# Performance work log

Measured on AMD Instinct MI355X. Metric: run time of the kernel, lower is better.

The kernel has to match this reference:

```python
import jax, jax.numpy as jnp
import numpy as np
from jax import lax

GROUPS = 8
EPS = 1e-5

def setup_inputs() -> dict:
    key = jax.random.key(0)
    ks = jax.random.split(key, 4)
    B, C, H, W = 32, 256, 64, 64
    cg = C // GROUPS  # 32 channels per group
    x = jax.random.normal(ks[0], (B, C, H, W), dtype=jnp.float32)
    w1 = jax.random.normal(ks[1], (cg, cg, 1, 1), dtype=jnp.float32) * 0.02  # conv1x1 OIHW
    b1 = jnp.zeros((cg,), jnp.float32)
    w3 = jax.random.normal(ks[2], (cg, cg, 3, 3), dtype=jnp.float32) * 0.02  # conv3x3 OIHW
    b3 = jnp.zeros((cg,), jnp.float32)
    gn_w = jnp.ones((cg,), jnp.float32)
    gn_b = jnp.zeros((cg,), jnp.float32)
    return {"x": x, "w1": w1, "b1": b1, "w3": w3, "b3": b3, "gn_w": gn_w, "gn_b": gn_b}

def reference(x, w1, b1, w3, b3, gn_w, gn_b):
    B, C, H, W = x.shape
    cg = C // GROUPS
    bg = B * GROUPS
    gx = x.reshape(bg, cg, H, W)

    # coordinate pooling: (bg,cg,H,1) and (bg,cg,W,1)
    x_h = jnp.mean(gx, axis=3, keepdims=True)
    x_w = jnp.mean(gx, axis=2, keepdims=True).transpose(0, 1, 3, 2)

    # 1x1 conv over concatenated coord features (bg,cg,H+W,1)
    hw = jnp.einsum('bihk,oi->bohk', jnp.concatenate([x_h, x_w], axis=2), w1[:, :, 0, 0])
    hw = hw + b1[None, :, None, None]
    xh, xw = hw[:, :, :H, :], hw[:, :, H:, :]

    # sigmoid coordinate gating
    gated = gx * jax.nn.sigmoid(xh) * jax.nn.sigmoid(xw.transpose(0, 1, 3, 2))

    # GroupNorm(cg groups over cg channels) == per-channel instance norm over HxW
    mu = jnp.mean(gated, axis=(2, 3), keepdims=True)
    var = jnp.var(gated, axis=(2, 3), keepdims=True)
    x1 = (gated - mu) * lax.rsqrt(var + EPS)
    x1 = x1 * gn_w[None, :, None, None] + gn_b[None, :, None, None]

    # 3x3 conv branch
    x2 = lax.conv_general_dilated(gx, w3, (1, 1), 'SAME',
                                  dimension_numbers=('NCHW', 'OIHW', 'NCHW'))
    x2 = x2 + b3[None, :, None, None]

    # cross-branch attention weights
    x11 = jax.nn.softmax(jnp.mean(x1, axis=(2, 3)), axis=-1)[:, None, :]  # (bg,1,cg)
    x21 = jax.nn.softmax(jnp.mean(x2, axis=(2, 3)), axis=-1)[:, None, :]  # (bg,1,cg)
    x12 = x2.reshape(bg, cg, H * W)
    x22 = x1.reshape(bg, cg, H * W)
    weights = (jnp.matmul(x11, x12) + jnp.matmul(x21, x22)).reshape(bg, 1, H, W)

    out = (gx * jax.nn.sigmoid(weights)).reshape(B, C, H, W) + x
    return out
```

## Files before the change

kernel.cpp:

```cpp
#include <hip/hip_runtime.h>
#include <math.h>

#define NPLANE 8192
#define PLANE  4096

__device__ __forceinline__ float sigm(float v){ return 1.0f/(1.0f+expf(-v)); }

__global__ __launch_bounds__(256) void kA(const float* __restrict__ x,
                                          float* __restrict__ rowsum,
                                          float* __restrict__ colsum,
                                          float* __restrict__ corners){
  const int plane = blockIdx.x;
  const float* __restrict__ p = x + (size_t)plane*PLANE;
  const int t = threadIdx.x;
  __shared__ float cpart[256][4];
  __shared__ float rsh[64];
  float ca0=0.f, ca1=0.f, ca2=0.f, ca3=0.f;
  #pragma unroll
  for(int iter=0; iter<4; ++iter){
    const int flat = iter*1024 + t*4;
    const float4 v = *reinterpret_cast<const float4*>(p + flat);
    float rp = v.x+v.y+v.z+v.w;
    #pragma unroll
    for(int s=1;s<16;s<<=1) rp += __shfl_xor(rp, s, 64);
    if((t&15)==0) rsh[flat>>6] = rp;
    ca0+=v.x; ca1+=v.y; ca2+=v.z; ca3+=v.w;
    if(iter==0 && t==0)   corners[(size_t)plane*4+0]=v.x;
    if(iter==0 && t==15)  corners[(size_t)plane*4+1]=v.w;
    if(iter==3 && t==240) corners[(size_t)plane*4+2]=v.x;
    if(iter==3 && t==255) corners[(size_t)plane*4+3]=v.w;
  }
  cpart[t][0]=ca0; cpart[t][1]=ca1; cpart[t][2]=ca2; cpart[t][3]=ca3;
  __syncthreads();
  if(t<64){
    const int g=t>>2, j=t&3;
    float s=0.f;
    #pragma unroll
    for(int k=0;k<16;++k) s += cpart[g + k*16][j];
    colsum[(size_t)plane*64 + t] = s;
    rowsum[(size_t)plane*64 + t] = rsh[t];
  }
}

__global__ __launch_bounds__(256) void kB0(const float* __restrict__ gn_b,
                                           const float* __restrict__ w3,
                                           const float* __restrict__ b3,
                                           float* __restrict__ wcg,
                                           float* __restrict__ cbg){
  __shared__ float x11[32];
  const int t=threadIdx.x;
  if(t==0){
    float m=-1e30f;
    #pragma unroll
    for(int c=0;c<32;++c) m=fmaxf(m,gn_b[c]);
    float e[32]; float s=0.f;
    #pragma unroll
    for(int c=0;c<32;++c){ e[c]=expf(gn_b[c]-m); s+=e[c]; }
    const float inv=1.f/s;
    float cb=0.f;
    #pragma unroll
    for(int c=0;c<32;++c){ x11[c]=e[c]*inv; cb+=x11[c]*b3[c]; }
    *cbg=cb;
  }
  __syncthreads();
  for(int idx=t; idx<288; idx+=256){
    const int i=idx/9, k=idx%9;
    float s=0.f;
    #pragma unroll
    for(int c=0;c<32;++c) s += x11[c]*w3[(c*32+i)*9+k];
    wcg[idx]=s;
  }
}

__global__ __launch_bounds__(256) void kB(const float* __restrict__ rowsum,
                                          const float* __restrict__ colsum,
                                          const float* __restrict__ corners,
                                          const float* __restrict__ w1,
                                          const float* __restrict__ b1,
                                          const float* __restrict__ w3,
                                          const float* __restrict__ b3,
                                          float* __restrict__ sh,
                                          float* __restrict__ sw,
                                          float* __restrict__ x21){
  const int b = blockIdx.x;
  const int t = threadIdx.x;
  __shared__ float m[32][128];
  __shared__ float w1s[1024];
  __shared__ float S[32][9];
  __shared__ float mean2[32];
  const float* __restrict__ rs = rowsum + (size_t)b*32*64;
  const float* __restrict__ cs = colsum + (size_t)b*32*64;
  for(int idx=t; idx<2048; idx+=256){
    m[idx>>6][idx&63]        = rs[idx]*(1.0f/64.0f);
    m[idx>>6][64+(idx&63)]   = cs[idx]*(1.0f/64.0f);
  }
  for(int idx=t; idx<1024; idx+=256) w1s[idx]=w1[idx];
  __syncthreads();
  {
    const int o = t>>3;
    const int p0 = (t&7)<<4;
    const float bias = b1[o];
    #pragma unroll
    for(int pp=0;pp<16;++pp){
      const int p = p0+pp;
      float acc = bias;
      #pragma unroll
      for(int i=0;i<32;++i) acc += w1s[o*32+i]*m[i][p];
      const float sg = sigm(acc);
      if(p<64) sh[((size_t)b*32+o)*64 + p]      = sg;
      else     sw[((size_t)b*32+o)*64 + (p-64)] = sg;
    }
  }
  if(t<32){
    const int i=t;
    float Ti=0.f;
    #pragma unroll
    for(int h=0;h<64;++h) Ti += m[i][h];
    Ti *= 64.f;
    const float r0=m[i][0]*64.f, r63=m[i][63]*64.f;
    const float c0=m[i][64]*64.f, c63=m[i][127]*64.f;
    const float* cr = corners + ((size_t)b*32+i)*4;
    const float k00=cr[0], k01=cr[1], k10=cr[2], k11=cr[3];
    #pragma unroll
    for(int ky=0;ky<3;++ky){
      #pragma unroll
      for(int kx=0;kx<3;++kx){
        float s=Ti;
        if(ky==0) s-=r63; else if(ky==2) s-=r0;
        if(kx==0) s-=c63; else if(kx==2) s-=c0;
        if(ky==0&&kx==0) s+=k11;
        if(ky==0&&kx==2) s+=k10;
        if(ky==2&&kx==0) s+=k01;
        if(ky==2&&kx==2) s+=k00;
        S[i][ky*3+kx]=s;
      }
    }
  }
  __syncthreads();
  if(t<32){
    const int c=t;
    float acc=0.f;
    for(int i=0;i<32;++i){
      #pragma unroll
      for(int k=0;k<9;++k) acc += w3[(c*32+i)*9+k]*S[i][k];
    }
    mean2[c] = acc*(1.0f/4096.0f) + b3[c];
  }
  __syncthreads();
  if(t==0){
    float mx=-1e30f;
    #pragma unroll
    for(int c=0;c<32;++c) mx=fmaxf(mx,mean2[c]);
    float e[32]; float s=0.f;
    #pragma unroll
    for(int c=0;c<32;++c){ e[c]=expf(mean2[c]-mx); s+=e[c]; }
    const float inv=1.f/s;
    #pragma unroll
    for(int c=0;c<32;++c) x21[(size_t)b*32+c]=e[c]*inv;
  }
}

__global__ __launch_bounds__(256) void kC(const float* __restrict__ x,
                                          const float* __restrict__ sh,
                                          const float* __restrict__ sw,
                                          float* __restrict__ musum,
                                          float* __restrict__ sqsum){
  const int plane = blockIdx.x;
  const int t = threadIdx.x;
  const float* __restrict__ p = x + (size_t)plane*PLANE;
  __shared__ float shs[64], sws[64];
  if(t<64){ shs[t]=sh[(size_t)plane*64+t]; sws[t]=sw[(size_t)plane*64+t]; }
  __syncthreads();
  float s=0.f, q=0.f;
  #pragma unroll
  for(int iter=0;iter<4;++iter){
    const int flat=iter*1024 + t*4;
    const float4 v = *reinterpret_cast<const float4*>(p+flat);
    const int row=flat>>6, col=flat&63;
    const float a=shs[row];
    const float g0=v.x*a*sws[col+0], g1=v.y*a*sws[col+1];
    const float g2=v.z*a*sws[col+2], g3=v.w*a*sws[col+3];
    s += g0+g1+g2+g3;
    q += g0*g0+g1*g1+g2*g2+g3*g3;
  }
  #pragma unroll
  for(int sft=1;sft<64;sft<<=1){ s+=__shfl_xor(s,sft,64); q+=__shfl_xor(q,sft,64); }
  __shared__ float rsum[4], rsq[4];
  if((t&63)==0){ rsum[t>>6]=s; rsq[t>>6]=q; }
  __syncthreads();
  if(t==0){ musum[plane]=rsum[0]+rsum[1]+rsum[2]+rsum[3];
            sqsum[plane]=rsq[0]+rsq[1]+rsq[2]+rsq[3]; }
}

__global__ __launch_bounds__(256) void kE(const float* __restrict__ x,
    const float* __restrict__ sh, const float* __restrict__ sw,
    const float* __restrict__ x21, const float* __restrict__ musum,
    const float* __restrict__ sqsum, const float* __restrict__ gn_w,
    const float* __restrict__ gn_b, const float* __restrict__ wc,
    const float* __restrict__ cb, float* __restrict__ out){
  const int b = blockIdx.x>>2;
  const int tile0 = (blockIdx.x&3)<<4;
  const int t = threadIdx.x;
  __shared__ float Lbuf[18][66];
  __shared__ float shs[32][16];
  __shared__ float sws[32][64];
  __shared__ float alphas[32];
  __shared__ float wcs[288];
  __shared__ float constsh;

  if(t<32){
    const float ms = musum[(size_t)b*32+t]*(1.0f/4096.0f);
    const float vv = sqsum[(size_t)b*32+t]*(1.0f/4096.0f) - ms*ms;
    const float rq = rsqrtf(vv + 1e-5f);
    const float xv = x21[(size_t)b*32+t];
    alphas[t] = xv*gn_w[t]*rq;
    float part = xv*(gn_b[t] - gn_w[t]*rq*ms);
    #pragma unroll
    for(int s=1;s<32;s<<=1) part += __shfl_xor(part, s, 64);
    if(t==0) constsh = part + cb[0];
  }
  for(int idx=t; idx<288; idx+=256) wcs[idx]=wc[idx];
  for(int idx=t; idx<512; idx+=256){
    const int i=idx>>4, r=idx&15;
    shs[i][r] = sh[((size_t)b*32+i)*64 + tile0 + r];
  }
  for(int idx=t; idx<2048; idx+=256){
    const int i=idx>>6, w=idx&63;
    sws[i][w] = sw[((size_t)b*32+i)*64 + w];
  }
  if(t<18){ Lbuf[t][0]=0.f; Lbuf[t][65]=0.f; }

  const int r  = t>>4;
  const int c0 = (t&15)<<2;
  float wacc0=0.f, wacc1=0.f, wacc2=0.f, wacc3=0.f;

  for(int i=0;i<32;++i){
    const float* __restrict__ p = x + ((size_t)b*32+i)*(size_t)PLANE;
    __syncthreads();
    for(int idx=t; idx<288; idx+=256){
      const int rr=idx>>4, c4=(idx&15)<<2;
      const int gr=tile0+rr-1;
      float4 v = make_float4(0.f,0.f,0.f,0.f);
      if(gr>=0 && gr<64) v = *reinterpret_cast<const float4*>(p + gr*64 + c4);
      Lbuf[rr][c4+1]=v.x; Lbuf[rr][c4+2]=v.y; Lbuf[rr][c4+3]=v.z; Lbuf[rr][c4+4]=v.w;
    }
    __syncthreads();
    const float q0=wcs[i*9+0], q1=wcs[i*9+1], q2=wcs[i*9+2];
    const float q3=wcs[i*9+3], q4=wcs[i*9+4], q5=wcs[i*9+5];
    const float q6=wcs[i*9+6], q7=wcs[i*9+7], q8=wcs[i*9+8];
    const float ash = alphas[i]*shs[i][r];
    #pragma unroll
    for(int j=0;j<4;++j){
      const int cc=c0+j+1;
      const float a0=Lbuf[r  ][cc-1], a1=Lbuf[r  ][cc], a2=Lbuf[r  ][cc+1];
      const float e0=Lbuf[r+1][cc-1], e1=Lbuf[r+1][cc], e2=Lbuf[r+1][cc+1];
      const float d0=Lbuf[r+2][cc-1], d1=Lbuf[r+2][cc], d2=Lbuf[r+2][cc+1];
      float acc = q0*a0+q1*a1+q2*a2 + q3*e0+q4*e1+q5*e2 + q6*d0+q7*d1+q8*d2;
      acc += ash*sws[i][c0+j]*e1;
      if(j==0) wacc0+=acc; else if(j==1) wacc1+=acc;
      else if(j==2) wacc2+=acc; else wacc3+=acc;
    }
  }
  __syncthreads();
  const float cst = constsh;
  const float wf0 = 1.f + sigm(wacc0+cst);
  const float wf1 = 1.f + sigm(wacc1+cst);
  const float wf2 = 1.f + sigm(wacc2+cst);
  const float wf3 = 1.f + sigm(wacc3+cst);
  const size_t rowoff = (size_t)(tile0+r)*64 + c0;
  for(int i=0;i<32;++i){
    const size_t off = ((size_t)b*32+i)*(size_t)PLANE + rowoff;
    const float4 v = *reinterpret_cast<const float4*>(x + off);
    float4 o;
    o.x=v.x*wf0; o.y=v.y*wf1; o.z=v.z*wf2; o.w=v.w*wf3;
    *reinterpret_cast<float4*>(out + off) = o;
  }
}

extern "C" void kernel_launch(void* const* d_in, const int* in_sizes, int n_in,
                              void* d_out, int out_size, void* d_ws, size_t ws_size,
                              hipStream_t stream){
  (void)in_sizes; (void)n_in; (void)out_size; (void)ws_size;
  const float* x    = (const float*)d_in[0];
  const float* w1   = (const float*)d_in[1];
  const float* b1   = (const float*)d_in[2];
  const float* w3   = (const float*)d_in[3];
  const float* b3   = (const float*)d_in[4];
  const float* gn_w = (const float*)d_in[5];
  const float* gn_b = (const float*)d_in[6];
  float* out = (float*)d_out;
  float* ws  = (float*)d_ws;

  float* rowsum  = ws + 0;
  float* colsum  = ws + 524288;
  float* corners = ws + 1048576;
  float* sh      = ws + 1081344;
  float* sw      = ws + 1605632;
  float* x21     = ws + 2129920;
  float* musum   = ws + 2138112;
  float* sqsum   = ws + 2146304;
  float* wc      = ws + 2154496;
  float* cb      = ws + 2154784;

  kA <<<NPLANE, 256, 0, stream>>>(x, rowsum, colsum, corners);
  kB0<<<1,      256, 0, stream>>>(gn_b, w3, b3, wc, cb);
  kB <<<256,    256, 0, stream>>>(rowsum, colsum, corners, w1, b1, w3, b3, sh, sw, x21);
  kC <<<NPLANE, 256, 0, stream>>>(x, sh, sw, musum, sqsum);
  kE <<<1024,   256, 0, stream>>>(x, sh, sw, x21, musum, sqsum, gn_w, gn_b, wc, cb, out);
}
```

Before: 353.9 us.

## Restructure conv-weight kernel to register-accumulate per-tap partials and drop per-channel barriers

The final kernel no longer stages an 18-row halo in shared memory with two barriers per input channel. Each thread now loads one float4 per channel straight from global memory and keeps 9-tap partial sums in registers. Those partials are combined across columns with lane shuffles and across rows through a small shared buffer, and the block grows to 320 threads to cover the halo rows. The stats kernels now issue all their loads up front, and the per-group kernel moves its w3 dot product and softmax onto all threads using transposed shared weights and wave shuffles. The cost is higher register pressure in the final kernel and extra idle threads outside the output rows.

New measurement: 343.6 us. -2.9%, faster.

```diff
diff --git a/kernel.cpp b/kernel.cpp
--- a/kernel.cpp
+++ b/kernel.cpp
@@ -13,22 +13,24 @@
   const int plane = blockIdx.x;
   const float* __restrict__ p = x + (size_t)plane*PLANE;
   const int t = threadIdx.x;
-  __shared__ float cpart[256][4];
+  __shared__ float cpart[256][5];
   __shared__ float rsh[64];
+  float4 v[4];
+  #pragma unroll
+  for(int it=0; it<4; ++it)
+    v[it] = *reinterpret_cast<const float4*>(p + it*1024 + t*4);
+  if(t==0)   corners[(size_t)plane*4+0]=v[0].x;
+  if(t==15)  corners[(size_t)plane*4+1]=v[0].w;
+  if(t==240) corners[(size_t)plane*4+2]=v[3].x;
+  if(t==255) corners[(size_t)plane*4+3]=v[3].w;
   float ca0=0.f, ca1=0.f, ca2=0.f, ca3=0.f;
   #pragma unroll
-  for(int iter=0; iter<4; ++iter){
-    const int flat = iter*1024 + t*4;
-    const float4 v = *reinterpret_cast<const float4*>(p + flat);
-    float rp = v.x+v.y+v.z+v.w;
+  for(int it=0; it<4; ++it){
+    float rp = v[it].x+v[it].y+v[it].z+v[it].w;
     #pragma unroll
     for(int s=1;s<16;s<<=1) rp += __shfl_xor(rp, s, 64);
-    if((t&15)==0) rsh[flat>>6] = rp;
-    ca0+=v.x; ca1+=v.y; ca2+=v.z; ca3+=v.w;
-    if(iter==0 && t==0)   corners[(size_t)plane*4+0]=v.x;
-    if(iter==0 && t==15)  corners[(size_t)plane*4+1]=v.w;
-    if(iter==3 && t==240) corners[(size_t)plane*4+2]=v.x;
-    if(iter==3 && t==255) corners[(size_t)plane*4+3]=v.w;
+    if((t&15)==0) rsh[it*16 + (t>>4)] = rp;
+    ca0+=v[it].x; ca1+=v[it].y; ca2+=v[it].z; ca3+=v[it].w;
   }
   cpart[t][0]=ca0; cpart[t][1]=ca1; cpart[t][2]=ca2; cpart[t][3]=ca3;
   __syncthreads();
@@ -84,41 +86,44 @@
                                           float* __restrict__ x21){
   const int b = blockIdx.x;
   const int t = threadIdx.x;
-  __shared__ float m[32][128];
-  __shared__ float w1s[1024];
-  __shared__ float S[32][9];
-  __shared__ float mean2[32];
-  const float* __restrict__ rs = rowsum + (size_t)b*32*64;
-  const float* __restrict__ cs = colsum + (size_t)b*32*64;
+  __shared__ float m[32*132];
+  __shared__ float w1t[1024];
+  __shared__ float w3t[9216];
+  __shared__ float sout[32*132];
+  __shared__ float S[288];
+  __shared__ float red[256];
+  const float* __restrict__ rs = rowsum + (size_t)b*2048;
+  const float* __restrict__ cs = colsum + (size_t)b*2048;
   for(int idx=t; idx<2048; idx+=256){
-    m[idx>>6][idx&63]        = rs[idx]*(1.0f/64.0f);
-    m[idx>>6][64+(idx&63)]   = cs[idx]*(1.0f/64.0f);
-  }
-  for(int idx=t; idx<1024; idx+=256) w1s[idx]=w1[idx];
+    const int i=idx>>6, h=idx&63;
+    m[i*132+h]    = rs[idx]*(1.0f/64.0f);
+    m[i*132+64+h] = cs[idx]*(1.0f/64.0f);
+  }
+  for(int idx=t; idx<1024; idx+=256) w1t[idx] = w1[(idx&31)*32 + (idx>>5)];
+  for(int idx=t; idx<9216; idx+=256){
+    const int c=idx&31, r=idx>>5, i=r/9, k=r-9*i;
+    w3t[idx] = w3[(c*32+i)*9+k];
+  }
   __syncthreads();
   {
-    const int o = t>>3;
-    const int p0 = (t&7)<<4;
-    const float bias = b1[o];
+    const int o = t&31, pg = t>>5;
+    const float bo = b1[o];
     #pragma unroll
     for(int pp=0;pp<16;++pp){
-      const int p = p0+pp;
-      float acc = bias;
-      #pragma unroll
-      for(int i=0;i<32;++i) acc += w1s[o*32+i]*m[i][p];
-      const float sg = sigm(acc);
-      if(p<64) sh[((size_t)b*32+o)*64 + p]      = sg;
-      else     sw[((size_t)b*32+o)*64 + (p-64)] = sg;
+      const int p = pg*16+pp;
+      float a = bo;
+      #pragma unroll
+      for(int i=0;i<32;++i) a += w1t[i*32+o]*m[i*132+p];
+      sout[o*132+p] = sigm(a);
     }
   }
   if(t<32){
     const int i=t;
     float Ti=0.f;
-    #pragma unroll
-    for(int h=0;h<64;++h) Ti += m[i][h];
+    for(int h=0;h<64;++h) Ti += m[i*132+h];
     Ti *= 64.f;
-    const float r0=m[i][0]*64.f, r63=m[i][63]*64.f;
-    const float c0=m[i][64]*64.f, c63=m[i][127]*64.f;
+    const float r0=m[i*132+0]*64.f, r63=m[i*132+63]*64.f;
+    const float c0=m[i*132+64]*64.f, c63=m[i*132+127]*64.f;
     const float* cr = corners + ((size_t)b*32+i)*4;
     const float k00=cr[0], k01=cr[1], k10=cr[2], k11=cr[3];
     #pragma unroll
@@ -132,31 +137,40 @@
         if(ky==0&&kx==2) s+=k10;
         if(ky==2&&kx==0) s+=k01;
         if(ky==2&&kx==2) s+=k00;
-        S[i][ky*3+kx]=s;
+        S[i*9+ky*3+kx]=s;
       }
     }
   }
   __syncthreads();
+  {
+    const int c = t&31, chunk = t>>5;
+    float part = 0.f;
+    #pragma unroll
+    for(int ii=0; ii<4; ++ii){
+      const int i = chunk*4+ii;
+      #pragma unroll
+      for(int k=0;k<9;++k) part += w3t[(i*9+k)*32+c]*S[i*9+k];
+    }
+    red[t] = part;
+  }
+  __syncthreads();
   if(t<32){
-    const int c=t;
-    float acc=0.f;
-    for(int i=0;i<32;++i){
-      #pragma unroll
-      for(int k=0;k<9;++k) acc += w3[(c*32+i)*9+k]*S[i][k];
-    }
-    mean2[c] = acc*(1.0f/4096.0f) + b3[c];
-  }
-  __syncthreads();
-  if(t==0){
-    float mx=-1e30f;
-    #pragma unroll
-    for(int c=0;c<32;++c) mx=fmaxf(mx,mean2[c]);
-    float e[32]; float s=0.f;
-    #pragma unroll
-    for(int c=0;c<32;++c){ e[c]=expf(mean2[c]-mx); s+=e[c]; }
-    const float inv=1.f/s;
-    #pragma unroll
-    for(int c=0;c<32;++c) x21[(size_t)b*32+c]=e[c]*inv;
+    float mm=0.f;
+    #pragma unroll
+    for(int ch=0;ch<8;++ch) mm += red[ch*32+t];
+    mm = mm*(1.0f/4096.0f) + b3[t];
+    float mx = mm;
+    #pragma unroll
+    for(int s=1;s<32;s<<=1) mx = fmaxf(mx, __shfl_xor(mx,s,64));
+    const float e = expf(mm-mx);
+    float ss = e;
+    #pragma unroll
+    for(int s=1;s<32;s<<=1) ss += __shfl_xor(ss,s,64);
+    x21[(size_t)b*32+t] = e/ss;
+  }
+  for(int idx=t; idx<2048; idx+=256){
+    sh[(size_t)b*2048+idx] = sout[(idx>>6)*132 + (idx&63)];
+    sw[(size_t)b*2048+idx] = sout[(idx>>6)*132 + 64 + (idx&63)];
   }
 }
 
@@ -169,17 +183,20 @@
   const int t = threadIdx.x;
   const float* __restrict__ p = x + (size_t)plane*PLANE;
   __shared__ float shs[64], sws[64];
+  float4 v[4];
+  #pragma unroll
+  for(int it=0;it<4;++it)
+    v[it] = *reinterpret_cast<const float4*>(p + it*1024 + t*4);
   if(t<64){ shs[t]=sh[(size_t)plane*64+t]; sws[t]=sw[(size_t)plane*64+t]; }
   __syncthreads();
+  const int col = (t&15)<<2;
+  const float4 swv = *reinterpret_cast<const float4*>(&sws[col]);
   float s=0.f, q=0.f;
   #pragma unroll
-  for(int iter=0;iter<4;++iter){
-    const int flat=iter*1024 + t*4;
-    const float4 v = *reinterpret_cast<const float4*>(p+flat);
-    const int row=flat>>6, col=flat&63;
-    const float a=shs[row];
-    const float g0=v.x*a*sws[col+0], g1=v.y*a*sws[col+1];
-    const float g2=v.z*a*sws[col+2], g3=v.w*a*sws[col+3];
+  for(int it=0;it<4;++it){
+    const float a = shs[it*16 + (t>>4)];
+    const float g0=v[it].x*a*swv.x, g1=v[it].y*a*swv.y;
+    const float g2=v[it].z*a*swv.z, g3=v[it].w*a*swv.w;
     s += g0+g1+g2+g3;
     q += g0*g0+g1*g1+g2*g2+g3*g3;
   }
@@ -192,7 +209,8 @@
             sqsum[plane]=rsq[0]+rsq[1]+rsq[2]+rsq[3]; }
 }
 
-__global__ __launch_bounds__(256) void kE(const float* __restrict__ x,
+#define TEB 320
+__global__ __launch_bounds__(TEB) void kE(const float* __restrict__ x,
     const float* __restrict__ sh, const float* __restrict__ sw,
     const float* __restrict__ x21, const float* __restrict__ musum,
     const float* __restrict__ sqsum, const float* __restrict__ gn_w,
@@ -201,11 +219,11 @@
   const int b = blockIdx.x>>2;
   const int tile0 = (blockIdx.x&3)<<4;
   const int t = threadIdx.x;
-  __shared__ float Lbuf[18][66];
-  __shared__ float shs[32][16];
-  __shared__ float sws[32][64];
+  __shared__ float H[3*18*68];
+  __shared__ float sws[32*64];
+  __shared__ float shs[32*16];
   __shared__ float alphas[32];
-  __shared__ float wcs[288];
+  __shared__ float wcs[292];
   __shared__ float constsh;
 
   if(t<32){
@@ -219,61 +237,79 @@
     for(int s=1;s<32;s<<=1) part += __shfl_xor(part, s, 64);
     if(t==0) constsh = part + cb[0];
   }
-  for(int idx=t; idx<288; idx+=256) wcs[idx]=wc[idx];
-  for(int idx=t; idx<512; idx+=256){
-    const int i=idx>>4, r=idx&15;
-    shs[i][r] = sh[((size_t)b*32+i)*64 + tile0 + r];
-  }
-  for(int idx=t; idx<2048; idx+=256){
-    const int i=idx>>6, w=idx&63;
-    sws[i][w] = sw[((size_t)b*32+i)*64 + w];
-  }
-  if(t<18){ Lbuf[t][0]=0.f; Lbuf[t][65]=0.f; }
-
-  const int r  = t>>4;
+  for(int idx=t; idx<288; idx+=TEB) wcs[idx]=wc[idx];
+  for(int idx=t; idx<512; idx+=TEB)
+    shs[idx] = sh[(size_t)b*2048 + (idx>>4)*64 + tile0 + (idx&15)];
+  for(int idx=t; idx<2048; idx+=TEB)
+    sws[idx] = sw[(size_t)b*2048 + idx];
+  __syncthreads();
+
+  const int hr = t>>4;
   const int c0 = (t&15)<<2;
-  float wacc0=0.f, wacc1=0.f, wacc2=0.f, wacc3=0.f;
-
-  for(int i=0;i<32;++i){
-    const float* __restrict__ p = x + ((size_t)b*32+i)*(size_t)PLANE;
-    __syncthreads();
-    for(int idx=t; idx<288; idx+=256){
-      const int rr=idx>>4, c4=(idx&15)<<2;
-      const int gr=tile0+rr-1;
+  const int gr = tile0 + hr - 1;
+  float acc[4][9];
+  float gacc[4];
+
+  if(t < 288){
+    #pragma unroll
+    for(int j=0;j<4;++j){
+      gacc[j]=0.f;
+      #pragma unroll
+      for(int k=0;k<9;++k) acc[j][k]=0.f;
+    }
+    const float rowmask = (hr>=1 && hr<=16) ? 1.f : 0.f;
+    const int   shi = min(max(hr-1,0),15);
+    const bool  inrow = (gr>=0) && (gr<64);
+    const float* __restrict__ px = x + ((size_t)b*32)*PLANE + (size_t)gr*64 + c0;
+    #pragma unroll 2
+    for(int i=0;i<32;++i){
       float4 v = make_float4(0.f,0.f,0.f,0.f);
-      if(gr>=0 && gr<64) v = *reinterpret_cast<const float4*>(p + gr*64 + c4);
-      Lbuf[rr][c4+1]=v.x; Lbuf[rr][c4+2]=v.y; Lbuf[rr][c4+3]=v.z; Lbuf[rr][c4+4]=v.w;
-    }
-    __syncthreads();
-    const float q0=wcs[i*9+0], q1=wcs[i*9+1], q2=wcs[i*9+2];
-    const float q3=wcs[i*9+3], q4=wcs[i*9+4], q5=wcs[i*9+5];
-    const float q6=wcs[i*9+6], q7=wcs[i*9+7], q8=wcs[i*9+8];
-    const float ash = alphas[i]*shs[i][r];
-    #pragma unroll
-    for(int j=0;j<4;++j){
-      const int cc=c0+j+1;
-      const float a0=Lbuf[r  ][cc-1], a1=Lbuf[r  ][cc], a2=Lbuf[r  ][cc+1];
-      const float e0=Lbuf[r+1][cc-1], e1=Lbuf[r+1][cc], e2=Lbuf[r+1][cc+1];
-      const float d0=Lbuf[r+2][cc-1], d1=Lbuf[r+2][cc], d2=Lbuf[r+2][cc+1];
-      float acc = q0*a0+q1*a1+q2*a2 + q3*e0+q4*e1+q5*e2 + q6*d0+q7*d1+q8*d2;
-      acc += ash*sws[i][c0+j]*e1;
-      if(j==0) wacc0+=acc; else if(j==1) wacc1+=acc;
-      else if(j==2) wacc2+=acc; else wacc3+=acc;
-    }
-  }
-  __syncthreads();
-  const float cst = constsh;
-  const float wf0 = 1.f + sigm(wacc0+cst);
-  const float wf1 = 1.f + sigm(wacc1+cst);
-  const float wf2 = 1.f + sigm(wacc2+cst);
-  const float wf3 = 1.f + sigm(wacc3+cst);
-  const size_t rowoff = (size_t)(tile0+r)*64 + c0;
-  for(int i=0;i<32;++i){
-    const size_t off = ((size_t)b*32+i)*(size_t)PLANE + rowoff;
-    const float4 v = *reinterpret_cast<const float4*>(x + off);
-    float4 o;
-    o.x=v.x*wf0; o.y=v.y*wf1; o.z=v.z*wf2; o.w=v.w*wf3;
-    *reinterpret_cast<float4*>(out + off) = o;
+      if(inrow) v = *reinterpret_cast<const float4*>(px + (size_t)i*PLANE);
+      const float ash = alphas[i]*shs[i*16+shi]*rowmask;
+      const float4 swv = *reinterpret_cast<const float4*>(&sws[i*64+c0]);
+      const float* __restrict__ wq = &wcs[i*9];
+      const float vv0=v.x, vv1=v.y, vv2=v.z, vv3=v.w;
+      #pragma unroll
+      for(int k=0;k<9;++k){
+        const float w = wq[k];
+        acc[0][k] += w*vv0; acc[1][k] += w*vv1;
+        acc[2][k] += w*vv2; acc[3][k] += w*vv3;
+      }
+      gacc[0] += ash*swv.x*vv0; gacc[1] += ash*swv.y*vv1;
+      gacc[2] += ash*swv.z*vv2; gacc[3] += ash*swv.w*vv3;
+    }
+    #pragma unroll
+    for(int ky=0;ky<3;++ky){
+      float lf = __shfl_up(acc[3][ky*3+0], 1);
+      float rt = __shfl_down(acc[0][ky*3+2], 1);
+      if(c0==0)  lf = 0.f;
+      if(c0==60) rt = 0.f;
+      const float h0 = lf             + acc[0][ky*3+1] + acc[1][ky*3+2];
+      const float h1 = acc[0][ky*3+0] + acc[1][ky*3+1] + acc[2][ky*3+2];
+      const float h2 = acc[1][ky*3+0] + acc[2][ky*3+1] + acc[3][ky*3+2];
+      const float h3 = acc[2][ky*3+0] + acc[3][ky*3+1] + rt;
+      *reinterpret_cast<float4*>(&H[(ky*18+hr)*68 + c0]) = make_float4(h0,h1,h2,h3);
+    }
+  }
+  __syncthreads();
+  if(t>=16 && t<272){
+    const float4 h0 = *reinterpret_cast<const float4*>(&H[(0*18 + hr-1)*68 + c0]);
+    const float4 h1 = *reinterpret_cast<const float4*>(&H[(1*18 + hr  )*68 + c0]);
+    const float4 h2 = *reinterpret_cast<const float4*>(&H[(2*18 + hr+1)*68 + c0]);
+    const float cst = constsh;
+    const float wf0 = 1.f + sigm(h0.x+h1.x+h2.x + gacc[0] + cst);
+    const float wf1 = 1.f + sigm(h0.y+h1.y+h2.y + gacc[1] + cst);
+    const float wf2 = 1.f + sigm(h0.z+h1.z+h2.z + gacc[2] + cst);
+    const float wf3 = 1.f + sigm(h0.w+h1.w+h2.w + gacc[3] + cst);
+    const float* __restrict__ px = x   + ((size_t)b*32)*PLANE + (size_t)gr*64 + c0;
+    float*       __restrict__ po = out + ((size_t)b*32)*PLANE + (size_t)gr*64 + c0;
+    #pragma unroll 4
+    for(int i=0;i<32;++i){
+      const float4 v = *reinterpret_cast<const float4*>(px + (size_t)i*PLANE);
+      float4 o;
+      o.x=v.x*wf0; o.y=v.y*wf1; o.z=v.z*wf2; o.w=v.w*wf3;
+      *reinterpret_cast<float4*>(po + (size_t)i*PLANE) = o;
+    }
   }
 }
 
@@ -306,5 +342,5 @@
   kB0<<<1,      256, 0, stream>>>(gn_b, w3, b3, wc, cb);
   kB <<<256,    256, 0, stream>>>(rowsum, colsum, corners, w1, b1, w3, b3, sh, sw, x21);
   kC <<<NPLANE, 256, 0, stream>>>(x, sh, sw, musum, sqsum);
-  kE <<<1024,   256, 0, stream>>>(x, sh, sw, x21, musum, sqsum, gn_w, gn_b, wc, cb, out);
-}
+  kE <<<1024,   TEB, 0, stream>>>(x, sh, sw, x21, musum, sqsum, gn_w, gn_b, wc, cb, out);
+}
```
